# Performance work log

Hardware: AMD Instinct MI355X
Metric: run time of the kernel (lower is better)

## Reference

```python
import jax, jax.numpy as jnp
import numpy as np

T, B, D, H = 1024, 64, 256, 256


def setup_inputs() -> dict:
    key = jax.random.key(0)
    ks = jax.random.split(key, 9)
    s = 1.0 / np.sqrt(D + H)  # roughly torch Linear init scale
    return {
        "inputs": jax.random.normal(ks[0], (T, B, D), dtype=jnp.float32),
        "Wf": jax.random.normal(ks[1], (H, D + H), dtype=jnp.float32) * s,
        "bf": jax.random.normal(ks[2], (H,), dtype=jnp.float32) * s,
        "Wi": jax.random.normal(ks[3], (H, D + H), dtype=jnp.float32) * s,
        "bi": jax.random.normal(ks[4], (H,), dtype=jnp.float32) * s,
        "Wg": jax.random.normal(ks[5], (H, D + H), dtype=jnp.float32) * s,
        "bg": jax.random.normal(ks[6], (H,), dtype=jnp.float32) * s,
        "Wo": jax.random.normal(ks[7], (H, D + H), dtype=jnp.float32) * s,
        "bo": jax.random.normal(ks[8], (H,), dtype=jnp.float32) * s,
    }


def reference(inputs, Wf, bf, Wi, bi, Wg, bg, Wo, bo):
    # inputs: [T, B, D]; torch Linear: y = x @ W.T + b
    Bsz = inputs.shape[1]
    h0 = jnp.zeros((Bsz, H), dtype=inputs.dtype)
    c0 = jnp.zeros((Bsz, H), dtype=inputs.dtype)

    def step(carry, x):
        hx, cx = carry
        comb = jnp.concatenate([x, hx], axis=1)  # [B, D+H]
        f = jax.nn.sigmoid(comb @ Wf.T + bf)
        i = jax.nn.sigmoid(comb @ Wi.T + bi)
        g = jnp.tanh(comb @ Wg.T + bg)
        o = jax.nn.sigmoid(comb @ Wo.T + bo)
        cx = f * cx + i * g
        hx = o * jnp.tanh(cx)
        return (hx, cx), hx

    (hx, cx), stacked = jax.lax.scan(step, (h0, c0), inputs)
    return stacked, hx, cx
```

## Files before the change

kernel.cpp:

```cpp
#include <hip/hip_runtime.h>
#include <cstdint>
#include <cstddef>

#define T_SEQ 1024
#define BATCH 64
#define DIM   256
#define HID   256
#define NG    (4*HID)

typedef _Float16 h2v __attribute__((ext_vector_type(2)));
union U16 { uint4 u; h2v h[4]; };

__device__ __forceinline__ float sigm_f(float x) {
    return 1.0f / (1.0f + __expf(-x));
}
__device__ __forceinline__ float tanh_f(float x) {
    x = fminf(fmaxf(x, -15.0f), 15.0f);
    float e = __expf(2.0f * x);
    return (e - 1.0f) / (e + 1.0f);
}

#define QP_XOR1(x) __int_as_float(__builtin_amdgcn_mov_dpp(__float_as_int(x), 0xB1, 0xf, 0xf, true))

__global__ void pack_kernel(const float* __restrict__ Wf, const float* __restrict__ bf,
                            const float* __restrict__ Wi, const float* __restrict__ bi,
                            const float* __restrict__ Wg, const float* __restrict__ bg,
                            const float* __restrict__ Wo, const float* __restrict__ bo,
                            float* __restrict__ wx4, _Float16* __restrict__ whB,
                            float* __restrict__ bias4,
                            float* __restrict__ hstate, float* __restrict__ cstate) {
    int k = blockIdx.x;
    int j = threadIdx.x;
    int r = j & 255, g = j >> 8;
    const float* W  = (g == 0) ? Wf : (g == 1) ? Wi : (g == 2) ? Wg : Wo;
    const float* bb = (g == 0) ? bf : (g == 1) ? bi : (g == 2) ? bg : bo;
    int jp = r * 4 + g;
    wx4[(size_t)k * 1024 + jp] = W[(size_t)r * 512 + k];
    {
        int k8 = k >> 3, e = k & 7, t = jp >> 1, s = jp & 1;
        whB[(((size_t)(k8 * 2 + s)) * 512 + t) * 8 + e] = (_Float16)W[(size_t)r * 512 + 256 + k];
    }
    if (k == 0) bias4[jp] = bb[r];
    if (k < 64 && g == 0) hstate[k * 256 + r] = 0.0f;
    if (k < 64 && g == 1) cstate[k * 256 + r] = 0.0f;
}

__global__ __launch_bounds__(256) void xproj_kernel(
        const float* __restrict__ X, const float* __restrict__ wx4,
        const float* __restrict__ bias4, float4* __restrict__ xp) {
    __shared__ __align__(16) float xl[256 * 20];
    int tid = threadIdx.x;
    int R0 = blockIdx.x * 16;
    #pragma unroll
    for (int i = 0; i < 16; ++i)
        xl[tid * 20 + i] = X[(size_t)(R0 + i) * DIM + tid];
    __syncthreads();

    float4 bv = ((const float4*)bias4)[tid];
    float acc[16][4];
    #pragma unroll
    for (int i = 0; i < 16; ++i) {
        acc[i][0] = bv.x; acc[i][1] = bv.y; acc[i][2] = bv.z; acc[i][3] = bv.w;
    }
    const float4* __restrict__ wp = (const float4*)wx4 + tid;
    #pragma unroll 2
    for (int k = 0; k < 256; ++k) {
        float4 w  = wp[k << 8];
        float4 xa = *(const float4*)&xl[k * 20 + 0];
        float4 xb = *(const float4*)&xl[k * 20 + 4];
        float4 xc = *(const float4*)&xl[k * 20 + 8];
        float4 xd = *(const float4*)&xl[k * 20 + 12];
        float xr[16] = {xa.x, xa.y, xa.z, xa.w, xb.x, xb.y, xb.z, xb.w,
                        xc.x, xc.y, xc.z, xc.w, xd.x, xd.y, xd.z, xd.w};
        #pragma unroll
        for (int i = 0; i < 16; ++i) {
            acc[i][0] = fmaf(xr[i], w.x, acc[i][0]);
            acc[i][1] = fmaf(xr[i], w.y, acc[i][1]);
            acc[i][2] = fmaf(xr[i], w.z, acc[i][2]);
            acc[i][3] = fmaf(xr[i], w.w, acc[i][3]);
        }
    }
    #pragma unroll
    for (int i = 0; i < 16; ++i) {
        float4 v;
        v.x = acc[i][0]; v.y = acc[i][1]; v.z = acc[i][2]; v.w = acc[i][3];
        xp[(size_t)(R0 + i) * 256 + tid] = v;
    }
}

__global__ __launch_bounds__(512, 2) void lstm_step_kernel(
        const float* __restrict__ xp, const _Float16* __restrict__ whB,
        float* __restrict__ hstate, float* __restrict__ cstate,
        float* __restrict__ out, int t0, int Tc) {
    __shared__ __align__(16) _Float16 wl[8 * 2 * 512 * 8];
    __shared__ __align__(16) _Float16 hl[2][HID];
    int t = threadIdx.x, b = blockIdx.x;

    {
        const uint4* src = (const uint4*)whB;
        uint4* dst = (uint4*)wl;
        #pragma unroll
        for (int i = 0; i < 16; ++i)
            dst[i * 512 + t] = src[i * 512 + t];
    }
    uint4 wr0[24], wr1[24];
    {
        const uint4* src = (const uint4*)whB;
        #pragma unroll
        for (int i = 0; i < 24; ++i) {
            wr0[i] = src[(size_t)((8 + i) * 2 + 0) * 512 + t];
            wr1[i] = src[(size_t)((8 + i) * 2 + 1) * 512 + t];
        }
    }
    int podd = t & 1;
    float creg = cstate[b * HID + (t >> 1)];
    if (t < HID) hl[0][t] = (_Float16)hstate[b * HID + t];
    float sm = podd ? 2.0f : 1.0f;
    float aa = podd ? 2.0f : 1.0f;
    float bbc = podd ? -1.0f : 0.0f;
    __syncthreads();

    const float2* __restrict__ xpf2 = (const float2*)xp;
    float2 xa2 = xpf2[((size_t)0 * BATCH + b) * 512 + t];
    int cur = 0;
    for (int tt = 0; tt < Tc; ++tt) {
        int tn = (tt + 1 < Tc) ? tt + 1 : tt;
        float2 xn2 = xpf2[((size_t)tn * BATCH + b) * 512 + t];

        float s0a = 0.f, s0b = 0.f, s1a = 0.f, s1b = 0.f;
        const _Float16* hb = hl[cur];
        #pragma unroll
        for (int k8 = 0; k8 < 8; ++k8) {
            U16 h, w0, w1;
            h.u  = *(const uint4*)&hb[k8 * 8];
            w0.u = *(const uint4*)&wl[((size_t)(k8 * 2 + 0) * 512 + t) * 8];
            w1.u = *(const uint4*)&wl[((size_t)(k8 * 2 + 1) * 512 + t) * 8];
            s0a = __builtin_amdgcn_fdot2(w0.h[0], h.h[0], s0a, false);
            s0b = __builtin_amdgcn_fdot2(w0.h[1], h.h[1], s0b, false);
            s0a = __builtin_amdgcn_fdot2(w0.h[2], h.h[2], s0a, false);
            s0b = __builtin_amdgcn_fdot2(w0.h[3], h.h[3], s0b, false);
            s1a = __builtin_amdgcn_fdot2(w1.h[0], h.h[0], s1a, false);
            s1b = __builtin_amdgcn_fdot2(w1.h[1], h.h[1], s1b, false);
            s1a = __builtin_amdgcn_fdot2(w1.h[2], h.h[2], s1a, false);
            s1b = __builtin_amdgcn_fdot2(w1.h[3], h.h[3], s1b, false);
        }
        #pragma unroll
        for (int i = 0; i < 24; ++i) {
            U16 h, w0, w1;
            h.u  = *(const uint4*)&hb[(8 + i) * 8];
            w0.u = wr0[i];
            w1.u = wr1[i];
            s0a = __builtin_amdgcn_fdot2(w0.h[0], h.h[0], s0a, false);
            s0b = __builtin_amdgcn_fdot2(w0.h[1], h.h[1], s0b, false);
            s0a = __builtin_amdgcn_fdot2(w0.h[2], h.h[2], s0a, false);
            s0b = __builtin_amdgcn_fdot2(w0.h[3], h.h[3], s0b, false);
            s1a = __builtin_amdgcn_fdot2(w1.h[0], h.h[0], s1a, false);
            s1b = __builtin_amdgcn_fdot2(w1.h[1], h.h[1], s1b, false);
            s1a = __builtin_amdgcn_fdot2(w1.h[2], h.h[2], s1a, false);
            s1b = __builtin_amdgcn_fdot2(w1.h[3], h.h[3], s1b, false);
        }
        float a0 = xa2.x + s0a + s0b;
        float a1 = xa2.y + s1a + s1b;
        float vA = fmaf(aa, sigm_f(sm * a0), bbc);
        float vB = sigm_f(a1);
        float eA = QP_XOR1(vA);
        float eB = QP_XOR1(vB);
        float f  = podd ? eA : vA;
        float ii = podd ? eB : vB;
        float gg = podd ? vA : eA;
        float o  = podd ? vB : eB;
        float c  = fmaf(f, creg, ii * gg);
        creg = c;
        float h  = o * tanh_f(c);
        if (!podd) hl[cur ^ 1][t >> 1] = (_Float16)h;
        __syncthreads();
        if (t < HID)
            out[((size_t)(t0 + tt) * BATCH + b) * HID + t] = (float)hl[cur ^ 1][t];
        xa2 = xn2;
        cur ^= 1;
    }
    if (t < HID) hstate[b * HID + t] = (float)hl[cur][t];
    if (!podd)   cstate[b * HID + (t >> 1)] = creg;
}

__global__ void tail_kernel(const float* __restrict__ hstate,
                            const float* __restrict__ cstate, float* __restrict__ out) {
    int b = blockIdx.x, r = threadIdx.x;
    size_t base = (size_t)T_SEQ * BATCH * HID;
    out[base + b * HID + r] = hstate[b * HID + r];
    out[base + (size_t)BATCH * HID + b * HID + r] = cstate[b * HID + r];
}

extern "C" void kernel_launch(void* const* d_in, const int* in_sizes, int n_in,
                              void* d_out, int out_size, void* d_ws, size_t ws_size,
                              hipStream_t stream) {
    (void)in_sizes; (void)n_in; (void)out_size;
    const float* X  = (const float*)d_in[0];
    const float* Wf = (const float*)d_in[1];
    const float* bf = (const float*)d_in[2];
    const float* Wi = (const float*)d_in[3];
    const float* bi = (const float*)d_in[4];
    const float* Wg = (const float*)d_in[5];
    const float* bg = (const float*)d_in[6];
    const float* Wo = (const float*)d_in[7];
    const float* bo = (const float*)d_in[8];
    float* out = (float*)d_out;
    char*  ws  = (char*)d_ws;

    const size_t MB = 1 << 20, KB = 1 << 10;
    float*    wx4    = (float*)(ws);
    _Float16* whB    = (_Float16*)(ws + MB);
    float*    bias4  = (float*)(ws + MB + 512 * KB);
    float*    hstate = (float*)(ws + MB + 576 * KB);
    float*    cstate = (float*)(ws + MB + 640 * KB);
    float4*   xproj  = (float4*)(ws + 2 * MB);

    size_t fixed = 2 * MB;
    int Tc = 1024;
    while (Tc > 16 && fixed + (size_t)Tc * BATCH * NG * 4 > ws_size) Tc >>= 1;

    pack_kernel<<<256, 1024, 0, stream>>>(Wf, bf, Wi, bi, Wg, bg, Wo, bo,
                                          wx4, whB, bias4, hstate, cstate);
    for (int t0 = 0; t0 < T_SEQ; t0 += Tc) {
        xproj_kernel<<<Tc * BATCH / 16, 256, 0, stream>>>(
            X + (size_t)t0 * BATCH * DIM, wx4, bias4, xproj);
        lstm_step_kernel<<<BATCH, 512, 0, stream>>>(
            (const float*)xproj, whB, hstate, cstate, out, t0, Tc);
    }
    tail_kernel<<<BATCH, HID, 0, stream>>>(hstate, cstate, out);
}
```

Before: 2.058 ms.

## Split each batch row's recurrence across two blocks exchanging partial sums via flags

The hidden-state reduction (K=256) for each batch row is now split across two workgroups, each holding half of the recurrent weights and half of h. The blocks trade partial dot products through a global buffer, with per-wave flag handshakes every timestep. Blocks are remapped so that paired halves land on the same XCD. This halves the per-thread weight registers and the dot-product work, and doubles the grid to 128 blocks, at the cost of a cross-block spin-wait and global-memory round trip on every step. It relies on both blocks of a pair being co-resident.

```diff
diff --git a/kernel.cpp b/kernel.cpp
--- a/kernel.cpp
+++ b/kernel.cpp
@@ -10,6 +10,7 @@
 
 typedef _Float16 h2v __attribute__((ext_vector_type(2)));
 union U16 { uint4 u; h2v h[4]; };
+union PU64 { float2 f2; unsigned long long u; };
 
 __device__ __forceinline__ float sigm_f(float x) {
     return 1.0f / (1.0f + __expf(-x));
@@ -28,7 +29,8 @@
                             const float* __restrict__ Wo, const float* __restrict__ bo,
                             float* __restrict__ wx4, _Float16* __restrict__ whB,
                             float* __restrict__ bias4,
-                            float* __restrict__ hstate, float* __restrict__ cstate) {
+                            float* __restrict__ hstate, float* __restrict__ cstate,
+                            unsigned* __restrict__ flags) {
     int k = blockIdx.x;
     int j = threadIdx.x;
     int r = j & 255, g = j >> 8;
@@ -37,12 +39,16 @@
     int jp = r * 4 + g;
     wx4[(size_t)k * 1024 + jp] = W[(size_t)r * 512 + k];
     {
-        int k8 = k >> 3, e = k & 7, t = jp >> 1, s = jp & 1;
-        whB[(((size_t)(k8 * 2 + s)) * 512 + t) * 8 + e] = (_Float16)W[(size_t)r * 512 + 256 + k];
+        int half = k >> 7, kk = k & 127;
+        int c = kk >> 3, e = k & 7;
+        int tcol = jp >> 1, s = jp & 1;
+        whB[(((size_t)((half * 16 + c) * 2 + s)) * 512 + tcol) * 8 + e] =
+            (_Float16)W[(size_t)r * 512 + 256 + k];
     }
     if (k == 0) bias4[jp] = bb[r];
     if (k < 64 && g == 0) hstate[k * 256 + r] = 0.0f;
     if (k < 64 && g == 1) cstate[k * 256 + r] = 0.0f;
+    if (k == 1 && j < 512) flags[j] = 0;
 }
 
 __global__ __launch_bounds__(256) void xproj_kernel(
@@ -91,50 +97,59 @@
 __global__ __launch_bounds__(512, 2) void lstm_step_kernel(
         const float* __restrict__ xp, const _Float16* __restrict__ whB,
         float* __restrict__ hstate, float* __restrict__ cstate,
-        float* __restrict__ out, int t0, int Tc) {
+        float* __restrict__ out, unsigned* __restrict__ flags,
+        float2* __restrict__ pbuf, int t0, int Tc) {
     __shared__ __align__(16) _Float16 wl[8 * 2 * 512 * 8];
-    __shared__ __align__(16) _Float16 hl[2][HID];
-    int t = threadIdx.x, b = blockIdx.x;
-
+    __shared__ __align__(16) _Float16 hl[2][128];
+    int t = threadIdx.x;
+    int orig = blockIdx.x;
+    int xcd = orig & 7, idx = orig >> 3;
+    int b = xcd * 8 + (idx >> 1);
+    int half = idx & 1;
+
+    const uint4* wsrc = (const uint4*)whB + (size_t)half * 16384;
     {
-        const uint4* src = (const uint4*)whB;
         uint4* dst = (uint4*)wl;
         #pragma unroll
         for (int i = 0; i < 16; ++i)
-            dst[i * 512 + t] = src[i * 512 + t];
-    }
-    uint4 wr0[24], wr1[24];
-    {
-        const uint4* src = (const uint4*)whB;
-        #pragma unroll
-        for (int i = 0; i < 24; ++i) {
-            wr0[i] = src[(size_t)((8 + i) * 2 + 0) * 512 + t];
-            wr1[i] = src[(size_t)((8 + i) * 2 + 1) * 512 + t];
-        }
-    }
+            dst[i * 512 + t] = wsrc[i * 512 + t];
+    }
+    uint4 wr0[8], wr1[8];
+    #pragma unroll
+    for (int i = 0; i < 8; ++i) {
+        wr0[i] = wsrc[(size_t)((8 + i) * 2 + 0) * 512 + t];
+        wr1[i] = wsrc[(size_t)((8 + i) * 2 + 1) * 512 + t];
+    }
+    int iskeep = (half == 0) ? (t < 256) : (t >= 256);
     int podd = t & 1;
-    float creg = cstate[b * HID + (t >> 1)];
-    if (t < HID) hl[0][t] = (_Float16)hstate[b * HID + t];
+    float creg = 0.0f;
+    if (iskeep) creg = cstate[b * HID + (t >> 1)];
+    if (t < 128) hl[0][t] = (_Float16)hstate[b * HID + half * 128 + t];
     float sm = podd ? 2.0f : 1.0f;
-    float aa = podd ? 2.0f : 1.0f;
-    float bbc = podd ? -1.0f : 0.0f;
+    float aa = sm, bbc = podd ? -1.0f : 0.0f;
     __syncthreads();
 
     const float2* __restrict__ xpf2 = (const float2*)xp;
-    float2 xa2 = xpf2[((size_t)0 * BATCH + b) * 512 + t];
+    float2 xa2 = {0.0f, 0.0f};
+    if (iskeep) xa2 = xpf2[(size_t)b * 512 + t];
+    int w4 = (t >> 6) & 3;
+    unsigned* flprod = &flags[(b * 2 + half) * 4 + w4];
+    unsigned* flcons = &flags[(b * 2 + (1 - half)) * 4 + w4];
     int cur = 0;
     for (int tt = 0; tt < Tc; ++tt) {
-        int tn = (tt + 1 < Tc) ? tt + 1 : tt;
-        float2 xn2 = xpf2[((size_t)tn * BATCH + b) * 512 + t];
-
+        float2 xn2 = xa2;
+        if (iskeep) {
+            int tn = (tt + 1 < Tc) ? tt + 1 : tt;
+            xn2 = xpf2[((size_t)tn * BATCH + b) * 512 + t];
+        }
         float s0a = 0.f, s0b = 0.f, s1a = 0.f, s1b = 0.f;
         const _Float16* hb = hl[cur];
         #pragma unroll
-        for (int k8 = 0; k8 < 8; ++k8) {
+        for (int c = 0; c < 8; ++c) {
             U16 h, w0, w1;
-            h.u  = *(const uint4*)&hb[k8 * 8];
-            w0.u = *(const uint4*)&wl[((size_t)(k8 * 2 + 0) * 512 + t) * 8];
-            w1.u = *(const uint4*)&wl[((size_t)(k8 * 2 + 1) * 512 + t) * 8];
+            h.u  = *(const uint4*)&hb[c * 8];
+            w0.u = *(const uint4*)&wl[((size_t)(c * 2 + 0) * 512 + t) * 8];
+            w1.u = *(const uint4*)&wl[((size_t)(c * 2 + 1) * 512 + t) * 8];
             s0a = __builtin_amdgcn_fdot2(w0.h[0], h.h[0], s0a, false);
             s0b = __builtin_amdgcn_fdot2(w0.h[1], h.h[1], s0b, false);
             s0a = __builtin_amdgcn_fdot2(w0.h[2], h.h[2], s0a, false);
@@ -145,7 +160,7 @@
             s1b = __builtin_amdgcn_fdot2(w1.h[3], h.h[3], s1b, false);
         }
         #pragma unroll
-        for (int i = 0; i < 24; ++i) {
+        for (int i = 0; i < 8; ++i) {
             U16 h, w0, w1;
             h.u  = *(const uint4*)&hb[(8 + i) * 8];
             w0.u = wr0[i];
@@ -159,28 +174,48 @@
             s1a = __builtin_amdgcn_fdot2(w1.h[2], h.h[2], s1a, false);
             s1b = __builtin_amdgcn_fdot2(w1.h[3], h.h[3], s1b, false);
         }
-        float a0 = xa2.x + s0a + s0b;
-        float a1 = xa2.y + s1a + s1b;
-        float vA = fmaf(aa, sigm_f(sm * a0), bbc);
-        float vB = sigm_f(a1);
-        float eA = QP_XOR1(vA);
-        float eB = QP_XOR1(vB);
-        float f  = podd ? eA : vA;
-        float ii = podd ? eB : vB;
-        float gg = podd ? vA : eA;
-        float o  = podd ? vB : eB;
-        float c  = fmaf(f, creg, ii * gg);
-        creg = c;
-        float h  = o * tanh_f(c);
-        if (!podd) hl[cur ^ 1][t >> 1] = (_Float16)h;
+        int parity = tt & 1;
+        if (!iskeep) {
+            PU64 p; p.f2.x = s0a + s0b; p.f2.y = s1a + s1b;
+            __hip_atomic_store(
+                (unsigned long long*)&pbuf[((size_t)(b * 2 + half) * 2 + parity) * 512 + t],
+                p.u, __ATOMIC_RELAXED, __HIP_MEMORY_SCOPE_AGENT);
+            asm volatile("s_waitcnt vmcnt(0)" ::: "memory");
+            if ((t & 63) == 0)
+                __hip_atomic_store(flprod, (unsigned)(t0 + tt + 1),
+                                   __ATOMIC_RELAXED, __HIP_MEMORY_SCOPE_AGENT);
+        } else {
+            unsigned want = (unsigned)(t0 + tt + 1);
+            while (__hip_atomic_load(flcons, __ATOMIC_RELAXED,
+                                     __HIP_MEMORY_SCOPE_AGENT) < want) {}
+            PU64 p;
+            p.u = __hip_atomic_load(
+                (const unsigned long long*)&pbuf[((size_t)(b * 2 + (1 - half)) * 2 + parity) * 512 + t],
+                __ATOMIC_RELAXED, __HIP_MEMORY_SCOPE_AGENT);
+            float a0 = xa2.x + s0a + s0b + p.f2.x;
+            float a1 = xa2.y + s1a + s1b + p.f2.y;
+            float vA = fmaf(aa, sigm_f(sm * a0), bbc);
+            float vB = sigm_f(a1);
+            float eA = QP_XOR1(vA);
+            float eB = QP_XOR1(vB);
+            float f  = podd ? eA : vA;
+            float ii = podd ? eB : vB;
+            float gg = podd ? vA : eA;
+            float o  = podd ? vB : eB;
+            float c  = fmaf(f, creg, ii * gg);
+            creg = c;
+            float h  = o * tanh_f(c);
+            if (!podd) hl[cur ^ 1][(t >> 1) & 127] = (_Float16)h;
+        }
         __syncthreads();
-        if (t < HID)
-            out[((size_t)(t0 + tt) * BATCH + b) * HID + t] = (float)hl[cur ^ 1][t];
+        if (t < 128)
+            out[((size_t)(t0 + tt) * BATCH + b) * HID + half * 128 + t] =
+                (float)hl[cur ^ 1][t];
         xa2 = xn2;
         cur ^= 1;
     }
-    if (t < HID) hstate[b * HID + t] = (float)hl[cur][t];
-    if (!podd)   cstate[b * HID + (t >> 1)] = creg;
+    if (t < 128) hstate[b * HID + half * 128 + t] = (float)hl[cur][t];
+    if (iskeep && !podd) cstate[b * HID + (t >> 1)] = creg;
 }
 
 __global__ void tail_kernel(const float* __restrict__ hstate,
@@ -213,19 +248,21 @@
     float*    bias4  = (float*)(ws + MB + 512 * KB);
     float*    hstate = (float*)(ws + MB + 576 * KB);
     float*    cstate = (float*)(ws + MB + 640 * KB);
-    float4*   xproj  = (float4*)(ws + 2 * MB);
-
-    size_t fixed = 2 * MB;
+    unsigned* flags  = (unsigned*)(ws + MB + 704 * KB);
+    float2*   pbuf   = (float2*)(ws + MB + 768 * KB);
+    float4*   xproj  = (float4*)(ws + 3 * MB);
+
+    size_t fixed = 3 * MB;
     int Tc = 1024;
     while (Tc > 16 && fixed + (size_t)Tc * BATCH * NG * 4 > ws_size) Tc >>= 1;
 
     pack_kernel<<<256, 1024, 0, stream>>>(Wf, bf, Wi, bi, Wg, bg, Wo, bo,
-                                          wx4, whB, bias4, hstate, cstate);
+                                          wx4, whB, bias4, hstate, cstate, flags);
     for (int t0 = 0; t0 < T_SEQ; t0 += Tc) {
         xproj_kernel<<<Tc * BATCH / 16, 256, 0, stream>>>(
             X + (size_t)t0 * BATCH * DIM, wx4, bias4, xproj);
-        lstm_step_kernel<<<BATCH, 512, 0, stream>>>(
-            (const float*)xproj, whB, hstate, cstate, out, t0, Tc);
+        lstm_step_kernel<<<128, 512, 0, stream>>>(
+            (const float*)xproj, whB, hstate, cstate, out, flags, pbuf, t0, Tc);
     }
     tail_kernel<<<BATCH, HID, 0, stream>>>(hstate, cstate, out);
 }
```

Result: slower. 4.311 ms (+109.5%).

## Split hidden-dim reduction across lane pairs to halve LDS h broadcast reads

Applied to the files above, without the earlier changes.

Restructures the recurrent matvec so each lane pair splits the K dimension in half. Each lane computes partial sums for all four gates of a hidden unit over 128 inputs instead of two gates over 256, and the halves are combined with a DPP cross-lane add. The weight packing is reordered to match, and the register-resident slice becomes 12x4 uint4. This halves the h vector loads from LDS per lane and keeps weight storage the same, at the cost of four extra DPP adds and a select per step.

```diff
diff --git a/kernel.cpp b/kernel.cpp
--- a/kernel.cpp
+++ b/kernel.cpp
@@ -37,8 +37,15 @@
     int jp = r * 4 + g;
     wx4[(size_t)k * 1024 + jp] = W[(size_t)r * 512 + k];
     {
-        int k8 = k >> 3, e = k & 7, t = jp >> 1, s = jp & 1;
-        whB[(((size_t)(k8 * 2 + s)) * 512 + t) * 8 + e] = (_Float16)W[(size_t)r * 512 + 256 + k];
+        int c = k >> 3, e = k & 7;
+        int R = jp >> 2, s = jp & 3;
+        int p = (c >= 16) ? 1 : 0;
+        int lc = c - 16 * p;
+        int t = 2 * R + p;
+        size_t idx = (lc < 4)
+            ? ((size_t)(lc * 4 + s) * 512 + t)
+            : (8192 + (size_t)((lc - 4) * 4 + s) * 512 + t);
+        whB[idx * 8 + e] = (_Float16)W[(size_t)r * 512 + 256 + k];
     }
     if (k == 0) bias4[jp] = bb[r];
     if (k < 64 && g == 0) hstate[k * 256 + r] = 0.0f;
@@ -92,7 +99,7 @@
         const float* __restrict__ xp, const _Float16* __restrict__ whB,
         float* __restrict__ hstate, float* __restrict__ cstate,
         float* __restrict__ out, int t0, int Tc) {
-    __shared__ __align__(16) _Float16 wl[8 * 2 * 512 * 8];
+    __shared__ __align__(16) _Float16 wl[16 * 512 * 8];
     __shared__ __align__(16) _Float16 hl[2][HID];
     int t = threadIdx.x, b = blockIdx.x;
 
@@ -103,64 +110,87 @@
         for (int i = 0; i < 16; ++i)
             dst[i * 512 + t] = src[i * 512 + t];
     }
-    uint4 wr0[24], wr1[24];
+    uint4 wrg[12][4];
     {
-        const uint4* src = (const uint4*)whB;
-        #pragma unroll
-        for (int i = 0; i < 24; ++i) {
-            wr0[i] = src[(size_t)((8 + i) * 2 + 0) * 512 + t];
-            wr1[i] = src[(size_t)((8 + i) * 2 + 1) * 512 + t];
-        }
+        const uint4* src = (const uint4*)whB + 8192;
+        #pragma unroll
+        for (int i = 0; i < 12; ++i)
+            #pragma unroll
+            for (int s = 0; s < 4; ++s)
+                wrg[i][s] = src[(size_t)((i * 4 + s) * 512) + t];
     }
     int podd = t & 1;
+    int cb = podd << 4;
     float creg = cstate[b * HID + (t >> 1)];
     if (t < HID) hl[0][t] = (_Float16)hstate[b * HID + t];
     float sm = podd ? 2.0f : 1.0f;
-    float aa = podd ? 2.0f : 1.0f;
-    float bbc = podd ? -1.0f : 0.0f;
+    float aa = sm, bbc = podd ? -1.0f : 0.0f;
     __syncthreads();
 
     const float2* __restrict__ xpf2 = (const float2*)xp;
-    float2 xa2 = xpf2[((size_t)0 * BATCH + b) * 512 + t];
+    float2 xa2 = xpf2[(size_t)b * 512 + t];
     int cur = 0;
     for (int tt = 0; tt < Tc; ++tt) {
         int tn = (tt + 1 < Tc) ? tt + 1 : tt;
         float2 xn2 = xpf2[((size_t)tn * BATCH + b) * 512 + t];
 
-        float s0a = 0.f, s0b = 0.f, s1a = 0.f, s1b = 0.f;
+        float sA0 = 0.f, sB0 = 0.f, sA1 = 0.f, sB1 = 0.f;
+        float sA2 = 0.f, sB2 = 0.f, sA3 = 0.f, sB3 = 0.f;
         const _Float16* hb = hl[cur];
         #pragma unroll
-        for (int k8 = 0; k8 < 8; ++k8) {
-            U16 h, w0, w1;
-            h.u  = *(const uint4*)&hb[k8 * 8];
-            w0.u = *(const uint4*)&wl[((size_t)(k8 * 2 + 0) * 512 + t) * 8];
-            w1.u = *(const uint4*)&wl[((size_t)(k8 * 2 + 1) * 512 + t) * 8];
-            s0a = __builtin_amdgcn_fdot2(w0.h[0], h.h[0], s0a, false);
-            s0b = __builtin_amdgcn_fdot2(w0.h[1], h.h[1], s0b, false);
-            s0a = __builtin_amdgcn_fdot2(w0.h[2], h.h[2], s0a, false);
-            s0b = __builtin_amdgcn_fdot2(w0.h[3], h.h[3], s0b, false);
-            s1a = __builtin_amdgcn_fdot2(w1.h[0], h.h[0], s1a, false);
-            s1b = __builtin_amdgcn_fdot2(w1.h[1], h.h[1], s1b, false);
-            s1a = __builtin_amdgcn_fdot2(w1.h[2], h.h[2], s1a, false);
-            s1b = __builtin_amdgcn_fdot2(w1.h[3], h.h[3], s1b, false);
+        for (int lc = 0; lc < 4; ++lc) {
+            U16 h; h.u = *(const uint4*)&hb[(cb + lc) * 8];
+            U16 w0, w1, w2, w3;
+            w0.u = *(const uint4*)&wl[((size_t)((lc * 4 + 0) * 512 + t)) * 8];
+            w1.u = *(const uint4*)&wl[((size_t)((lc * 4 + 1) * 512 + t)) * 8];
+            w2.u = *(const uint4*)&wl[((size_t)((lc * 4 + 2) * 512 + t)) * 8];
+            w3.u = *(const uint4*)&wl[((size_t)((lc * 4 + 3) * 512 + t)) * 8];
+            sA0 = __builtin_amdgcn_fdot2(w0.h[0], h.h[0], sA0, false);
+            sB0 = __builtin_amdgcn_fdot2(w0.h[1], h.h[1], sB0, false);
+            sA0 = __builtin_amdgcn_fdot2(w0.h[2], h.h[2], sA0, false);
+            sB0 = __builtin_amdgcn_fdot2(w0.h[3], h.h[3], sB0, false);
+            sA1 = __builtin_amdgcn_fdot2(w1.h[0], h.h[0], sA1, false);
+            sB1 = __builtin_amdgcn_fdot2(w1.h[1], h.h[1], sB1, false);
+            sA1 = __builtin_amdgcn_fdot2(w1.h[2], h.h[2], sA1, false);
+            sB1 = __builtin_amdgcn_fdot2(w1.h[3], h.h[3], sB1, false);
+            sA2 = __builtin_amdgcn_fdot2(w2.h[0], h.h[0], sA2, false);
+            sB2 = __builtin_amdgcn_fdot2(w2.h[1], h.h[1], sB2, false);
+            sA2 = __builtin_amdgcn_fdot2(w2.h[2], h.h[2], sA2, false);
+            sB2 = __builtin_amdgcn_fdot2(w2.h[3], h.h[3], sB2, false);
+            sA3 = __builtin_amdgcn_fdot2(w3.h[0], h.h[0], sA3, false);
+            sB3 = __builtin_amdgcn_fdot2(w3.h[1], h.h[1], sB3, false);
+            sA3 = __builtin_amdgcn_fdot2(w3.h[2], h.h[2], sA3, false);
+            sB3 = __builtin_amdgcn_fdot2(w3.h[3], h.h[3], sB3, false);
         }
         #pragma unroll
-        for (int i = 0; i < 24; ++i) {
-            U16 h, w0, w1;
-            h.u  = *(const uint4*)&hb[(8 + i) * 8];
-            w0.u = wr0[i];
-            w1.u = wr1[i];
-            s0a = __builtin_amdgcn_fdot2(w0.h[0], h.h[0], s0a, false);
-            s0b = __builtin_amdgcn_fdot2(w0.h[1], h.h[1], s0b, false);
-            s0a = __builtin_amdgcn_fdot2(w0.h[2], h.h[2], s0a, false);
-            s0b = __builtin_amdgcn_fdot2(w0.h[3], h.h[3], s0b, false);
-            s1a = __builtin_amdgcn_fdot2(w1.h[0], h.h[0], s1a, false);
-            s1b = __builtin_amdgcn_fdot2(w1.h[1], h.h[1], s1b, false);
-            s1a = __builtin_amdgcn_fdot2(w1.h[2], h.h[2], s1a, false);
-            s1b = __builtin_amdgcn_fdot2(w1.h[3], h.h[3], s1b, false);
+        for (int i = 0; i < 12; ++i) {
+            U16 h; h.u = *(const uint4*)&hb[(cb + 4 + i) * 8];
+            U16 w0, w1, w2, w3;
+            w0.u = wrg[i][0]; w1.u = wrg[i][1]; w2.u = wrg[i][2]; w3.u = wrg[i][3];
+            sA0 = __builtin_amdgcn_fdot2(w0.h[0], h.h[0], sA0, false);
+            sB0 = __builtin_amdgcn_fdot2(w0.h[1], h.h[1], sB0, false);
+            sA0 = __builtin_amdgcn_fdot2(w0.h[2], h.h[2], sA0, false);
+            sB0 = __builtin_amdgcn_fdot2(w0.h[3], h.h[3], sB0, false);
+            sA1 = __builtin_amdgcn_fdot2(w1.h[0], h.h[0], sA1, false);
+            sB1 = __builtin_amdgcn_fdot2(w1.h[1], h.h[1], sB1, false);
+            sA1 = __builtin_amdgcn_fdot2(w1.h[2], h.h[2], sA1, false);
+            sB1 = __builtin_amdgcn_fdot2(w1.h[3], h.h[3], sB1, false);
+            sA2 = __builtin_amdgcn_fdot2(w2.h[0], h.h[0], sA2, false);
+            sB2 = __builtin_amdgcn_fdot2(w2.h[1], h.h[1], sB2, false);
+            sA2 = __builtin_amdgcn_fdot2(w2.h[2], h.h[2], sA2, false);
+            sB2 = __builtin_amdgcn_fdot2(w2.h[3], h.h[3], sB2, false);
+            sA3 = __builtin_amdgcn_fdot2(w3.h[0], h.h[0], sA3, false);
+            sB3 = __builtin_amdgcn_fdot2(w3.h[1], h.h[1], sB3, false);
+            sA3 = __builtin_amdgcn_fdot2(w3.h[2], h.h[2], sA3, false);
+            sB3 = __builtin_amdgcn_fdot2(w3.h[3], h.h[3], sB3, false);
         }
-        float a0 = xa2.x + s0a + s0b;
-        float a1 = xa2.y + s1a + s1b;
+        float P0 = sA0 + sB0, P1 = sA1 + sB1, P2 = sA2 + sB2, P3 = sA3 + sB3;
+        float S0 = P0 + QP_XOR1(P0);
+        float S1 = P1 + QP_XOR1(P1);
+        float S2 = P2 + QP_XOR1(P2);
+        float S3 = P3 + QP_XOR1(P3);
+        float a0 = xa2.x + (podd ? S2 : S0);
+        float a1 = xa2.y + (podd ? S3 : S1);
         float vA = fmaf(aa, sigm_f(sm * a0), bbc);
         float vB = sigm_f(a1);
         float eA = QP_XOR1(vA);
```

Result: no change. 2.069 ms (+0.6%).
